# Performance work log

Measured on AMD Instinct MI355X. Metric: run time of the kernel, lower is better.

The kernel has to match this reference:

```python
import jax, jax.numpy as jnp
import numpy as np

B, N, H, L, DK, DV = 16, 325, 8, 24, 64, 64


def setup_inputs() -> dict:
    key = jax.random.key(0)
    k1, k2, k3, k4, k5 = jax.random.split(key, 5)
    Q = jax.random.normal(k1, (B, N, H, L, DK), dtype=jnp.float32)
    K = jax.random.normal(k2, (B, N, H, L, DK), dtype=jnp.float32)
    V = jax.random.normal(k3, (B, N, H, L, DV), dtype=jnp.float32)
    attn_mask = jax.random.uniform(k4, (B, N, H, L, L), dtype=jnp.float32)
    res_att = jax.random.normal(k5, (B, N, H, L, L), dtype=jnp.float32)
    return {"Q": Q, "K": K, "V": V, "attn_mask": attn_mask, "res_att": res_att}


def reference(Q, K, V, attn_mask, res_att):
    d_k = Q.shape[-1]
    inv_sqrt_dk = 1.0 / np.sqrt(d_k).astype(np.float32)
    # scores: [B, N, H, len_q, len_k]
    scores = jnp.einsum('bnhqd,bnhkd->bnhqk', Q, K) * inv_sqrt_dk + res_att
    # in-place masked_fill_ in the original mutates scores before return
    scores = jnp.where(attn_mask > 0.5, jnp.float32(-1e9), scores)
    # NOTE: original softmaxes over dim=3, the len_q axis of the 5-D scores
    attn = jax.nn.softmax(scores, axis=3)
    context = jnp.einsum('bnhqk,bnhkv->bnhqv', attn, V)
    return (context, scores)
```

## Files before the change

### kernel.cpp

```cpp
#include <hip/hip_runtime.h>
#include <math.h>

#define NB   16
#define NN   325
#define NH   8
#define LL   24
#define DK   64
#define DV   64
#define NG   (NB * NN * NH)
#define STR  68
#define SSTR 25

__device__ __forceinline__ float dot4(float4 a, float4 b) {
    return a.x * b.x + a.y * b.y + a.z * b.z + a.w * b.w;
}

__global__ __launch_bounds__(256) void tatt_kernel(
    const float* __restrict__ Q, const float* __restrict__ K,
    const float* __restrict__ V, const float* __restrict__ Mask,
    const float* __restrict__ Res, float* __restrict__ outC,
    float* __restrict__ outS)
{
    __shared__ float sQ[LL * STR];
    __shared__ float sK[LL * STR];
    __shared__ float sV[LL * STR];
    __shared__ float sS[LL * SSTR];
    __shared__ float sM[LL];
    __shared__ float sI[LL];

    const int g   = blockIdx.x;
    const int tid = threadIdx.x;

    const float* Qg = Q    + (size_t)g * (LL * DK);
    const float* Kg = K    + (size_t)g * (LL * DK);
    const float* Vg = V    + (size_t)g * (LL * DV);
    const float* Mg = Mask + (size_t)g * (LL * LL);
    const float* Rg = Res  + (size_t)g * (LL * LL);
    float*       Cg = outC + (size_t)g * (LL * DV);
    float*       Sg = outS + (size_t)g * (LL * LL);

    #pragma unroll
    for (int ii = 0; ii < 5; ++ii) {
        int i = tid + ii * 256;
        if (i < 1152) {
            int m   = i / 384;
            int j   = i - m * 384;
            int row = j >> 4;
            int c   = (j & 15) << 2;
            const float* src = (m == 0) ? Qg : (m == 1) ? Kg : Vg;
            float*       dst = (m == 0) ? sQ : (m == 1) ? sK : sV;
            float4 val = *(const float4*)(src + row * DK + c);
            *(float4*)(dst + row * STR + c) = val;
        }
    }
    __syncthreads();

    if (tid < 64) {
        const int q0 = (tid >> 3) * 3;
        const int k0 = (tid & 7) * 3;
        float acc[3][3] = {{0.f,0.f,0.f},{0.f,0.f,0.f},{0.f,0.f,0.f}};
        for (int d = 0; d < DK; d += 4) {
            float4 qv0 = *(const float4*)(sQ + (q0 + 0) * STR + d);
            float4 qv1 = *(const float4*)(sQ + (q0 + 1) * STR + d);
            float4 qv2 = *(const float4*)(sQ + (q0 + 2) * STR + d);
            float4 kv0 = *(const float4*)(sK + (k0 + 0) * STR + d);
            float4 kv1 = *(const float4*)(sK + (k0 + 1) * STR + d);
            float4 kv2 = *(const float4*)(sK + (k0 + 2) * STR + d);
            acc[0][0] += dot4(qv0, kv0); acc[0][1] += dot4(qv0, kv1); acc[0][2] += dot4(qv0, kv2);
            acc[1][0] += dot4(qv1, kv0); acc[1][1] += dot4(qv1, kv1); acc[1][2] += dot4(qv1, kv2);
            acc[2][0] += dot4(qv2, kv0); acc[2][1] += dot4(qv2, kv1); acc[2][2] += dot4(qv2, kv2);
        }
        #pragma unroll
        for (int r = 0; r < 3; ++r) {
            #pragma unroll
            for (int c = 0; c < 3; ++c) {
                int q = q0 + r, k = k0 + c;
                float s = acc[r][c] * 0.125f + Rg[q * LL + k];
                s = (Mg[q * LL + k] > 0.5f) ? -1e9f : s;
                sS[q * SSTR + k] = s;
            }
        }
    }
    __syncthreads();

    if (tid < 144) {
        int i0 = tid * 4;
        float4 o;
        {
            int i = i0 + 0; int q = i / LL, k = i - q * LL; o.x = sS[q * SSTR + k];
        }
        {
            int i = i0 + 1; int q = i / LL, k = i - q * LL; o.y = sS[q * SSTR + k];
        }
        {
            int i = i0 + 2; int q = i / LL, k = i - q * LL; o.z = sS[q * SSTR + k];
        }
        {
            int i = i0 + 3; int q = i / LL, k = i - q * LL; o.w = sS[q * SSTR + k];
        }
        *(float4*)(Sg + i0) = o;
    } else if (tid >= 192 && tid < 192 + LL) {
        int k = tid - 192;
        float m = -INFINITY;
        #pragma unroll
        for (int q = 0; q < LL; ++q) m = fmaxf(m, sS[q * SSTR + k]);
        float sum = 0.f;
        #pragma unroll
        for (int q = 0; q < LL; ++q) sum += __expf(sS[q * SSTR + k] - m);
        sM[k] = m;
        sI[k] = 1.f / sum;
    }
    __syncthreads();

    #pragma unroll
    for (int ii = 0; ii < 3; ++ii) {
        int i = tid + ii * 256;
        if (i < LL * LL) {
            int q = i / LL, k = i - q * LL;
            sS[q * SSTR + k] = __expf(sS[q * SSTR + k] - sM[k]) * sI[k];
        }
    }
    __syncthreads();

    if (tid < 192) {
        const int q0 = (tid >> 4) * 2;
        const int v0 = (tid & 15) * 4;
        float4 acc0 = {0.f, 0.f, 0.f, 0.f};
        float4 acc1 = {0.f, 0.f, 0.f, 0.f};
        for (int k = 0; k < LL; ++k) {
            float a0 = sS[(q0 + 0) * SSTR + k];
            float a1 = sS[(q0 + 1) * SSTR + k];
            float4 vv = *(const float4*)(sV + k * STR + v0);
            acc0.x += a0 * vv.x; acc0.y += a0 * vv.y; acc0.z += a0 * vv.z; acc0.w += a0 * vv.w;
            acc1.x += a1 * vv.x; acc1.y += a1 * vv.y; acc1.z += a1 * vv.z; acc1.w += a1 * vv.w;
        }
        *(float4*)(Cg + (q0 + 0) * DV + v0) = acc0;
        *(float4*)(Cg + (q0 + 1) * DV + v0) = acc1;
    }
}

extern "C" void kernel_launch(void* const* d_in, const int* in_sizes, int n_in,
                              void* d_out, int out_size, void* d_ws, size_t ws_size,
                              hipStream_t stream) {
    const float* Q    = (const float*)d_in[0];
    const float* K    = (const float*)d_in[1];
    const float* V    = (const float*)d_in[2];
    const float* Mask = (const float*)d_in[3];
    const float* Res  = (const float*)d_in[4];
    float* outC = (float*)d_out;
    float* outS = (float*)d_out + (size_t)NG * LL * DV;
    hipLaunchKernelGGL(tatt_kernel, dim3(NG), dim3(256), 0, stream,
                       Q, K, V, Mask, Res, outC, outS);
}
```

Measured before the change: 930.4 us.

## Use single-wavefront blocks reading Q/K/V directly from global memory

Shrinks each block from 256 threads to one 64-lane wavefront and drops the shared-memory staging of Q, K and V. QK^T and PV now read operands straight from global memory. Scale, residual and mask are applied with vectorized float4 loads and stores, and the column softmax reduction is split across lane pairs with shuffles. The aim is to cut LDS traffic, barrier cost and idle threads so more blocks fit per CU, at the cost of repeated global/L1 reads of Q, K and V.

```diff
diff --git a/kernel.cpp b/kernel.cpp
--- a/kernel.cpp
+++ b/kernel.cpp
@@ -8,28 +8,24 @@
 #define DK   64
 #define DV   64
 #define NG   (NB * NN * NH)
-#define STR  68
-#define SSTR 25
+#define SSTR 28
 
 __device__ __forceinline__ float dot4(float4 a, float4 b) {
     return a.x * b.x + a.y * b.y + a.z * b.z + a.w * b.w;
 }
 
-__global__ __launch_bounds__(256) void tatt_kernel(
+__global__ __launch_bounds__(64) void tatt_kernel(
     const float* __restrict__ Q, const float* __restrict__ K,
     const float* __restrict__ V, const float* __restrict__ Mask,
     const float* __restrict__ Res, float* __restrict__ outC,
     float* __restrict__ outS)
 {
-    __shared__ float sQ[LL * STR];
-    __shared__ float sK[LL * STR];
-    __shared__ float sV[LL * STR];
-    __shared__ float sS[LL * SSTR];
-    __shared__ float sM[LL];
-    __shared__ float sI[LL];
+    __shared__ __align__(16) float sS[LL * SSTR];
+    __shared__ __align__(16) float sM[LL];
+    __shared__ __align__(16) float sI[LL];
 
-    const int g   = blockIdx.x;
-    const int tid = threadIdx.x;
+    const int g    = blockIdx.x;
+    const int lane = threadIdx.x;
 
     const float* Qg = Q    + (size_t)g * (LL * DK);
     const float* Kg = K    + (size_t)g * (LL * DK);
@@ -39,103 +35,128 @@
     float*       Cg = outC + (size_t)g * (LL * DV);
     float*       Sg = outS + (size_t)g * (LL * LL);
 
-    #pragma unroll
-    for (int ii = 0; ii < 5; ++ii) {
-        int i = tid + ii * 256;
-        if (i < 1152) {
-            int m   = i / 384;
-            int j   = i - m * 384;
-            int row = j >> 4;
-            int c   = (j & 15) << 2;
-            const float* src = (m == 0) ? Qg : (m == 1) ? Kg : Vg;
-            float*       dst = (m == 0) ? sQ : (m == 1) ? sK : sV;
-            float4 val = *(const float4*)(src + row * DK + c);
-            *(float4*)(dst + row * STR + c) = val;
+    {
+        const int q0 = (lane >> 3) * 3;
+        const int k0 = (lane & 7) * 3;
+        const float* qp = Qg + q0 * DK;
+        const float* kp = Kg + k0 * DK;
+        float a00 = 0.f, a01 = 0.f, a02 = 0.f;
+        float a10 = 0.f, a11 = 0.f, a12 = 0.f;
+        float a20 = 0.f, a21 = 0.f, a22 = 0.f;
+        #pragma unroll 4
+        for (int d = 0; d < DK; d += 4) {
+            float4 qv0 = *(const float4*)(qp + d);
+            float4 qv1 = *(const float4*)(qp + DK + d);
+            float4 qv2 = *(const float4*)(qp + 2 * DK + d);
+            float4 kv0 = *(const float4*)(kp + d);
+            float4 kv1 = *(const float4*)(kp + DK + d);
+            float4 kv2 = *(const float4*)(kp + 2 * DK + d);
+            a00 += dot4(qv0, kv0); a01 += dot4(qv0, kv1); a02 += dot4(qv0, kv2);
+            a10 += dot4(qv1, kv0); a11 += dot4(qv1, kv1); a12 += dot4(qv1, kv2);
+            a20 += dot4(qv2, kv0); a21 += dot4(qv2, kv1); a22 += dot4(qv2, kv2);
+        }
+        float* p0 = sS + (q0 + 0) * SSTR + k0;
+        float* p1 = sS + (q0 + 1) * SSTR + k0;
+        float* p2 = sS + (q0 + 2) * SSTR + k0;
+        p0[0] = a00; p0[1] = a01; p0[2] = a02;
+        p1[0] = a10; p1[1] = a11; p1[2] = a12;
+        p2[0] = a20; p2[1] = a21; p2[2] = a22;
+    }
+    __syncthreads();
+
+    float4 s40, s41, s42 = make_float4(0.f, 0.f, 0.f, 0.f);
+    #define PHASE_B(I0, DST) { \
+        const int i0_ = (I0); \
+        const int q_ = i0_ / 24, kk_ = i0_ - q_ * 24; \
+        float4 p_  = *(const float4*)(sS + q_ * SSTR + kk_); \
+        float4 r_  = *(const float4*)(Rg + i0_); \
+        float4 mm_ = *(const float4*)(Mg + i0_); \
+        float4 s_; \
+        s_.x = (mm_.x > 0.5f) ? -1e9f : fmaf(p_.x, 0.125f, r_.x); \
+        s_.y = (mm_.y > 0.5f) ? -1e9f : fmaf(p_.y, 0.125f, r_.y); \
+        s_.z = (mm_.z > 0.5f) ? -1e9f : fmaf(p_.z, 0.125f, r_.z); \
+        s_.w = (mm_.w > 0.5f) ? -1e9f : fmaf(p_.w, 0.125f, r_.w); \
+        *(float4*)(Sg + i0_) = s_; \
+        *(float4*)(sS + q_ * SSTR + kk_) = s_; \
+        DST = s_; }
+
+    PHASE_B(lane * 4, s40);
+    PHASE_B(lane * 4 + 256, s41);
+    if (lane < 16) { PHASE_B(lane * 4 + 512, s42); }
+    __syncthreads();
+
+    if (lane < 48) {
+        const int k = lane >> 1;
+        const float* cp = sS + (lane & 1) * (12 * SSTR) + k;
+        float vv[12];
+        #pragma unroll
+        for (int j = 0; j < 12; ++j) vv[j] = cp[j * SSTR];
+        float m = vv[0];
+        #pragma unroll
+        for (int j = 1; j < 12; ++j) m = fmaxf(m, vv[j]);
+        m = fmaxf(m, __shfl_xor(m, 1));
+        float sum = 0.f;
+        #pragma unroll
+        for (int j = 0; j < 12; ++j) sum += __expf(vv[j] - m);
+        sum += __shfl_xor(sum, 1);
+        if ((lane & 1) == 0) {
+            sM[k] = m;
+            sI[k] = 1.f / sum;
         }
     }
     __syncthreads();
 
-    if (tid < 64) {
-        const int q0 = (tid >> 3) * 3;
-        const int k0 = (tid & 7) * 3;
-        float acc[3][3] = {{0.f,0.f,0.f},{0.f,0.f,0.f},{0.f,0.f,0.f}};
-        for (int d = 0; d < DK; d += 4) {
-            float4 qv0 = *(const float4*)(sQ + (q0 + 0) * STR + d);
-            float4 qv1 = *(const float4*)(sQ + (q0 + 1) * STR + d);
-            float4 qv2 = *(const float4*)(sQ + (q0 + 2) * STR + d);
-            float4 kv0 = *(const float4*)(sK + (k0 + 0) * STR + d);
-            float4 kv1 = *(const float4*)(sK + (k0 + 1) * STR + d);
-            float4 kv2 = *(const float4*)(sK + (k0 + 2) * STR + d);
-            acc[0][0] += dot4(qv0, kv0); acc[0][1] += dot4(qv0, kv1); acc[0][2] += dot4(qv0, kv2);
-            acc[1][0] += dot4(qv1, kv0); acc[1][1] += dot4(qv1, kv1); acc[1][2] += dot4(qv1, kv2);
-            acc[2][0] += dot4(qv2, kv0); acc[2][1] += dot4(qv2, kv1); acc[2][2] += dot4(qv2, kv2);
-        }
-        #pragma unroll
-        for (int r = 0; r < 3; ++r) {
-            #pragma unroll
-            for (int c = 0; c < 3; ++c) {
-                int q = q0 + r, k = k0 + c;
-                float s = acc[r][c] * 0.125f + Rg[q * LL + k];
-                s = (Mg[q * LL + k] > 0.5f) ? -1e9f : s;
-                sS[q * SSTR + k] = s;
-            }
-        }
-    }
+    #define PHASE_D(I0, SV) { \
+        const int i0_ = (I0); \
+        const int q_ = i0_ / 24, kk_ = i0_ - q_ * 24; \
+        float4 m_ = *(const float4*)(sM + kk_); \
+        float4 j_ = *(const float4*)(sI + kk_); \
+        float4 a_; \
+        a_.x = __expf(SV.x - m_.x) * j_.x; \
+        a_.y = __expf(SV.y - m_.y) * j_.y; \
+        a_.z = __expf(SV.z - m_.z) * j_.z; \
+        a_.w = __expf(SV.w - m_.w) * j_.w; \
+        *(float4*)(sS + q_ * SSTR + kk_) = a_; }
+
+    PHASE_D(lane * 4, s40);
+    PHASE_D(lane * 4 + 256, s41);
+    if (lane < 16) { PHASE_D(lane * 4 + 512, s42); }
     __syncthreads();
 
-    if (tid < 144) {
-        int i0 = tid * 4;
-        float4 o;
-        {
-            int i = i0 + 0; int q = i / LL, k = i - q * LL; o.x = sS[q * SSTR + k];
+    {
+        const int v0c = (lane & 15) * 4;
+        const int qb  = (lane >> 4) * 6;
+        const float* sA = sS + qb * SSTR;
+        float4 o0 = {0,0,0,0}, o1 = {0,0,0,0}, o2 = {0,0,0,0};
+        float4 o3 = {0,0,0,0}, o4 = {0,0,0,0}, o5 = {0,0,0,0};
+        #define PV_STEP(COMP, J) { \
+            float4 vv = *(const float4*)(vp + (J) * DV); \
+            o0.x += a0.COMP * vv.x; o0.y += a0.COMP * vv.y; o0.z += a0.COMP * vv.z; o0.w += a0.COMP * vv.w; \
+            o1.x += a1.COMP * vv.x; o1.y += a1.COMP * vv.y; o1.z += a1.COMP * vv.z; o1.w += a1.COMP * vv.w; \
+            o2.x += a2.COMP * vv.x; o2.y += a2.COMP * vv.y; o2.z += a2.COMP * vv.z; o2.w += a2.COMP * vv.w; \
+            o3.x += a3.COMP * vv.x; o3.y += a3.COMP * vv.y; o3.z += a3.COMP * vv.z; o3.w += a3.COMP * vv.w; \
+            o4.x += a4.COMP * vv.x; o4.y += a4.COMP * vv.y; o4.z += a4.COMP * vv.z; o4.w += a4.COMP * vv.w; \
+            o5.x += a5.COMP * vv.x; o5.y += a5.COMP * vv.y; o5.z += a5.COMP * vv.z; o5.w += a5.COMP * vv.w; }
+        #pragma unroll
+        for (int kk = 0; kk < LL; kk += 4) {
+            float4 a0 = *(const float4*)(sA + 0 * SSTR + kk);
+            float4 a1 = *(const float4*)(sA + 1 * SSTR + kk);
+            float4 a2 = *(const float4*)(sA + 2 * SSTR + kk);
+            float4 a3 = *(const float4*)(sA + 3 * SSTR + kk);
+            float4 a4 = *(const float4*)(sA + 4 * SSTR + kk);
+            float4 a5 = *(const float4*)(sA + 5 * SSTR + kk);
+            const float* vp = Vg + kk * DV + v0c;
+            PV_STEP(x, 0)
+            PV_STEP(y, 1)
+            PV_STEP(z, 2)
+            PV_STEP(w, 3)
         }
-        {
-            int i = i0 + 1; int q = i / LL, k = i - q * LL; o.y = sS[q * SSTR + k];
-        }
-        {
-            int i = i0 + 2; int q = i / LL, k = i - q * LL; o.z = sS[q * SSTR + k];
-        }
-        {
-            int i = i0 + 3; int q = i / LL, k = i - q * LL; o.w = sS[q * SSTR + k];
-        }
-        *(float4*)(Sg + i0) = o;
-    } else if (tid >= 192 && tid < 192 + LL) {
-        int k = tid - 192;
-        float m = -INFINITY;
-        #pragma unroll
-        for (int q = 0; q < LL; ++q) m = fmaxf(m, sS[q * SSTR + k]);
-        float sum = 0.f;
-        #pragma unroll
-        for (int q = 0; q < LL; ++q) sum += __expf(sS[q * SSTR + k] - m);
-        sM[k] = m;
-        sI[k] = 1.f / sum;
-    }
-    __syncthreads();
-
-    #pragma unroll
-    for (int ii = 0; ii < 3; ++ii) {
-        int i = tid + ii * 256;
-        if (i < LL * LL) {
-            int q = i / LL, k = i - q * LL;
-            sS[q * SSTR + k] = __expf(sS[q * SSTR + k] - sM[k]) * sI[k];
-        }
-    }
-    __syncthreads();
-
-    if (tid < 192) {
-        const int q0 = (tid >> 4) * 2;
-        const int v0 = (tid & 15) * 4;
-        float4 acc0 = {0.f, 0.f, 0.f, 0.f};
-        float4 acc1 = {0.f, 0.f, 0.f, 0.f};
-        for (int k = 0; k < LL; ++k) {
-            float a0 = sS[(q0 + 0) * SSTR + k];
-            float a1 = sS[(q0 + 1) * SSTR + k];
-            float4 vv = *(const float4*)(sV + k * STR + v0);
-            acc0.x += a0 * vv.x; acc0.y += a0 * vv.y; acc0.z += a0 * vv.z; acc0.w += a0 * vv.w;
-            acc1.x += a1 * vv.x; acc1.y += a1 * vv.y; acc1.z += a1 * vv.z; acc1.w += a1 * vv.w;
-        }
-        *(float4*)(Cg + (q0 + 0) * DV + v0) = acc0;
-        *(float4*)(Cg + (q0 + 1) * DV + v0) = acc1;
+        *(float4*)(Cg + (qb + 0) * DV + v0c) = o0;
+        *(float4*)(Cg + (qb + 1) * DV + v0c) = o1;
+        *(float4*)(Cg + (qb + 2) * DV + v0c) = o2;
+        *(float4*)(Cg + (qb + 3) * DV + v0c) = o3;
+        *(float4*)(Cg + (qb + 4) * DV + v0c) = o4;
+        *(float4*)(Cg + (qb + 5) * DV + v0c) = o5;
     }
 }
 
@@ -149,6 +170,6 @@
     const float* Res  = (const float*)d_in[4];
     float* outC = (float*)d_out;
     float* outS = (float*)d_out + (size_t)NG * LL * DV;
-    hipLaunchKernelGGL(tatt_kernel, dim3(NG), dim3(256), 0, stream,
+    hipLaunchKernelGGL(tatt_kernel, dim3(NG), dim3(64), 0, stream,
                        Q, K, V, Mask, Res, outC, outS);
 }
```

Result: slower. 998.0 us (+7.3%).
